# Performance work log

Hardware: AMD Instinct MI355X
Metric: run time of the kernel (lower is better)

## Reference

```python
import jax, jax.numpy as jnp
import numpy as np
import math

B, S, D, H, MAX_LEN = 4, 1024, 1024, 16, 1024
DH = D // H  # 64

def setup_inputs() -> dict:
    key = jax.random.key(0)
    ks = jax.random.split(key, 9)
    s = 1.0 / math.sqrt(D)
    return {
        "q":  jax.random.normal(ks[0], (B, S, D), jnp.float32),
        "kv": jax.random.normal(ks[1], (B, S, D), jnp.float32),
        "Wq": jax.random.normal(ks[2], (D, D), jnp.float32) * s,
        "bq": jax.random.normal(ks[3], (D,), jnp.float32) * s,
        "Wk": jax.random.normal(ks[4], (D, D), jnp.float32) * s,
        "bk": jax.random.normal(ks[5], (D,), jnp.float32) * s,
        "Wv": jax.random.normal(ks[6], (D, D), jnp.float32) * s,
        "bv": jax.random.normal(ks[7], (D,), jnp.float32) * s,
        "Er": jax.random.normal(ks[8], (MAX_LEN, DH), jnp.float32),
    }

def _skew(QEr):
    # QEr: [B, H, S, S]. Music-Transformer skew trick:
    # pad one zero column on the left, reshape, drop first row.
    b, h, r, c = QEr.shape
    padded = jnp.pad(QEr, ((0, 0), (0, 0), (0, 0), (1, 0)))  # [b,h,r,c+1]
    reshaped = padded.reshape(b, h, c + 1, r)
    return reshaped[:, :, 1:, :]  # [b,h,r,c]

def reference(q, kv, Wq, bq, Wk, bk, Wv, bv, Er):
    b, s, d = kv.shape
    # projections (nn.Linear: x @ W + b with W stored [in,out])
    k = (kv @ Wk + bk).reshape(b, s, H, DH).transpose(0, 2, 3, 1)  # [b,h,dh,s]
    v = (kv @ Wv + bv).reshape(b, s, H, DH).transpose(0, 2, 1, 3)  # [b,h,s,dh]
    qh = (q @ Wq + bq).reshape(b, s, H, DH).transpose(0, 2, 1, 3)  # [b,h,s,dh]
    # relative position scores
    Er_t = Er[MAX_LEN - s:, :].T            # [dh, s]
    QEr = jnp.einsum('bhsd,dt->bhst', qh, Er_t)
    Srel = _skew(QEr)                        # [b,h,s,s]
    # content scores
    QK = jnp.einsum('bhsd,bhdt->bhst', qh, k)
    attn = (QK + Srel) / math.sqrt(DH)
    causal = jnp.tril(jnp.ones((s, s), dtype=bool))[None, None]
    attn = jnp.where(causal, attn, -jnp.inf)
    attn = jax.nn.softmax(attn, axis=-1)
    out = jnp.einsum('bhst,bhtd->bhsd', attn, v)
    out = out.transpose(0, 2, 1, 3).reshape(b, s, d)
    return out  # dropout is identity (p=0 / eval)
```

## Files before the change

kernel.cpp:

```cpp
#include <hip/hip_runtime.h>
#include <hip/hip_bf16.h>

typedef __bf16 bf16x8 __attribute__((ext_vector_type(8)));
typedef __bf16 bf16x4 __attribute__((ext_vector_type(4)));
typedef float  f32x4  __attribute__((ext_vector_type(4)));

#define MFMA_B16(a, b, c) __builtin_amdgcn_mfma_f32_16x16x32_bf16((a), (b), (c), 0, 0, 0)

static constexpr int Bk  = 4;
static constexpr int Sk  = 1024;
static constexpr int Dk  = 1024;
static constexpr int Hk  = 16;
static constexpr int DHk = 64;

static constexpr size_t QH_OFF = 0;
static constexpr size_t K_OFF  = 4194304;
static constexpr size_t VT_OFF = 8388608;
static constexpr size_t WT_OFF = 12582912;
static constexpr size_t ER_OFF = 15728640;
static constexpr size_t WS_ELEMS = 15794176;

__device__ __forceinline__ void load_lds16(const void* g, void* l) {
    __builtin_amdgcn_global_load_lds((const __attribute__((address_space(1))) void*)g,
                                     (__attribute__((address_space(3))) void*)l, 16, 0, 0);
}

__global__ void prep_kernel(const float* __restrict__ Wq, const float* __restrict__ Wk,
                            const float* __restrict__ Wv, const float* __restrict__ Er,
                            __bf16* __restrict__ wt, __bf16* __restrict__ erb)
{
    __shared__ float tile[64][65];
    const int z = blockIdx.z;
    const int tid = threadIdx.x;
    if (z == 3) {
        int idx = (blockIdx.y * 16 + blockIdx.x) * 256 + tid;
        erb[idx] = (__bf16)Er[idx];
        return;
    }
    const float* W = (z == 0) ? Wq : (z == 1 ? Wk : Wv);
    __bf16* dst = wt + (size_t)z * Dk * Dk;
    const int k0 = blockIdx.y * 64, n0 = blockIdx.x * 64;
    #pragma unroll
    for (int j = 0; j < 16; ++j) {
        int idx = tid + j * 256; int r = idx >> 6, c = idx & 63;
        tile[r][c] = W[(size_t)(k0 + r) * Dk + n0 + c];
    }
    __syncthreads();
    #pragma unroll
    for (int j = 0; j < 16; ++j) {
        int idx = tid + j * 256; int r = idx >> 6, c = idx & 63;
        dst[(size_t)(n0 + r) * Dk + k0 + c] = (__bf16)tile[c][r];
    }
}

__global__ __launch_bounds__(256) void proj_kernel(
    const float* __restrict__ Xq, const float* __restrict__ Xkv,
    const float* __restrict__ bq, const float* __restrict__ bk,
    const float* __restrict__ bv, const __bf16* __restrict__ wt,
    __bf16* __restrict__ qh, __bf16* __restrict__ kws, __bf16* __restrict__ vt)
{
    __shared__ __align__(16) float  Al[128 * 32];
    __shared__ __align__(16) __bf16 Bl[128 * 32];

    const int z = blockIdx.z;
    const float* X    = (z == 0) ? Xq : Xkv;
    const float* bias = (z == 0) ? bq : (z == 1 ? bk : bv);
    const __bf16* Wz  = wt + (size_t)z * Dk * Dk;

    const int m0   = blockIdx.x * 128;
    const int n0   = blockIdx.y * 128;
    const int tid  = threadIdx.x;
    const int lane = tid & 63;
    const int w    = tid >> 6;
    const int wr   = w >> 1, wc = w & 1;
    const int l15  = lane & 15;
    const int g    = lane >> 4;

    const float* asrc[4];
    int adst[4];
    #pragma unroll
    for (int i = 0; i < 4; ++i) {
        const int c = w * 4 + i;
        asrc[i] = X + (size_t)(m0 + c * 8 + (lane >> 3)) * Dk + (((lane & 7) ^ (lane >> 3)) << 2);
        adst[i] = c * 1024 + lane * 16;
    }
    const __bf16* bsrc[2];
    int bdst[2];
    #pragma unroll
    for (int i = 0; i < 2; ++i) {
        const int c = w * 2 + i;
        bsrc[i] = Wz + (size_t)(n0 + c * 16 + (lane >> 2)) * Dk + (((lane & 3) ^ ((lane >> 3) & 3)) << 3);
        bdst[i] = c * 1024 + lane * 16;
    }

    int aoff0[4], aoff1[4], boff[4];
    #pragma unroll
    for (int m = 0; m < 4; ++m) {
        const int row = wr * 64 + m * 16 + l15;
        aoff0[m] = row * 128 + (((2 * g)     ^ (l15 & 7)) << 4);
        aoff1[m] = row * 128 + (((2 * g + 1) ^ (l15 & 7)) << 4);
    }
    #pragma unroll
    for (int n = 0; n < 4; ++n) {
        const int row = wc * 64 + n * 16 + l15;
        boff[n] = row * 64 + ((g ^ ((l15 >> 1) & 3)) << 4);
    }

    const f32x4 fz = {0.f, 0.f, 0.f, 0.f};
    f32x4 acc[4][4];
    #pragma unroll
    for (int m = 0; m < 4; ++m)
        #pragma unroll
        for (int n = 0; n < 4; ++n) acc[m][n] = fz;

    const char* Alc = (const char*)Al;
    const char* Blc = (const char*)Bl;

    for (int ks = 0; ks < Dk / 32; ++ks) {
        #pragma unroll
        for (int i = 0; i < 4; ++i)
            load_lds16(asrc[i], (char*)Al + adst[i]);
        #pragma unroll
        for (int i = 0; i < 2; ++i)
            load_lds16(bsrc[i], (char*)Bl + bdst[i]);
        #pragma unroll
        for (int i = 0; i < 4; ++i) asrc[i] += 32;
        #pragma unroll
        for (int i = 0; i < 2; ++i) bsrc[i] += 32;
        __syncthreads();

        bf16x8 bf[4];
        #pragma unroll
        for (int n = 0; n < 4; ++n)
            bf[n] = *(const bf16x8*)(Blc + boff[n]);
        bf16x8 af[4];
        #pragma unroll
        for (int m = 0; m < 4; ++m) {
            f32x4 x0 = *(const f32x4*)(Alc + aoff0[m]);
            f32x4 x1 = *(const f32x4*)(Alc + aoff1[m]);
            bf16x8 a;
            a[0] = (__bf16)x0[0]; a[1] = (__bf16)x0[1]; a[2] = (__bf16)x0[2]; a[3] = (__bf16)x0[3];
            a[4] = (__bf16)x1[0]; a[5] = (__bf16)x1[1]; a[6] = (__bf16)x1[2]; a[7] = (__bf16)x1[3];
            af[m] = a;
        }

        #pragma unroll
        for (int m = 0; m < 4; ++m)
            #pragma unroll
            for (int n = 0; n < 4; ++n)
                acc[m][n] = MFMA_B16(af[m], bf[n], acc[m][n]);
        __syncthreads();
    }

    #pragma unroll
    for (int n = 0; n < 4; ++n) {
        const float bb = bias[n0 + wc * 64 + n * 16 + l15];
        #pragma unroll
        for (int m = 0; m < 4; ++m)
            #pragma unroll
            for (int r = 0; r < 4; ++r) acc[m][n][r] += bb;
    }

    const int b   = m0 >> 10;
    const int s0t = (m0 & 1023) + wr * 64;
    const int h   = (n0 + wc * 64) >> 6;

    if (z < 2) {
        __bf16* dst = (z == 0) ? qh : kws;
        const size_t rowbase = (size_t)(b * Hk + h) * Sk;
        #pragma unroll
        for (int m = 0; m < 4; ++m) {
            #pragma unroll
            for (int r = 0; r < 4; ++r) {
                const int s = s0t + m * 16 + g * 4 + r;
                __bf16* drow = dst + (rowbase + s) * DHk;
                #pragma unroll
                for (int n = 0; n < 4; ++n)
                    drow[n * 16 + l15] = (__bf16)acc[m][n][r];
            }
        }
    } else {
        const size_t hb = (size_t)(b * Hk + h) * DHk;
        #pragma unroll
        for (int m = 0; m < 4; ++m) {
            const int sb = s0t + m * 16 + g * 4;
            #pragma unroll
            for (int n = 0; n < 4; ++n) {
                const int dh = n * 16 + l15;
                bf16x4 pk;
                #pragma unroll
                for (int r = 0; r < 4; ++r) pk[r] = (__bf16)acc[m][n][r];
                *(bf16x4*)(vt + (hb + dh) * Sk + sb) = pk;
            }
        }
    }
}

__global__ __launch_bounds__(256, 3) void attn_kernel(
    const __bf16* __restrict__ qh, const __bf16* __restrict__ kws,
    const __bf16* __restrict__ vt, const __bf16* __restrict__ erb,
    float* __restrict__ out)
{
    __shared__ __align__(16) __bf16 Kl[2][4096];
    __shared__ __align__(16) __bf16 Vl[2][4096];
    __shared__ __align__(16) __bf16 P_lds[4][16][88];

    const int tid  = threadIdx.x;
    const int lane = tid & 63;
    const int w    = tid >> 6;
    const int l15  = lane & 15;
    const int g    = lane >> 4;

    const int lid   = blockIdx.x;
    const int bh    = lid & 63;
    const int strip = 15 - (lid >> 6);
    const int ntw   = strip + 1;
    const int sw    = strip * 64 + w * 16;

    const __bf16* kbase = kws + (size_t)bh * Sk * DHk;
    const __bf16* vbase = vt  + (size_t)bh * DHk * Sk;
    const __bf16* qbase = qh  + ((size_t)bh * Sk + sw) * DHk;

    __bf16 (*Pw)[88] = P_lds[w];

    const int trow   = tid >> 3;
    const int tslot  = tid & 7;
    const int srcoff = (tslot ^ (trow & 7)) << 3;
    char* kd0 = (char*)Kl + tid * 16;
    char* vd0 = (char*)Vl + tid * 16;

    bf16x8 aq[2];
    aq[0] = *(const bf16x8*)(qbase + l15 * DHk + g * 8);
    aq[1] = *(const bf16x8*)(qbase + l15 * DHk + 32 + g * 8);

    const f32x4 fz = {0.f, 0.f, 0.f, 0.f};
    f32x4 O[4];
    float m_[4], l_[4];
    #pragma unroll
    for (int n = 0; n < 4; ++n) O[n] = fz;
    #pragma unroll
    for (int r = 0; r < 4; ++r) { m_[r] = -1e30f; l_[r] = 0.f; }

    load_lds16(kbase + (size_t)trow * DHk + srcoff,        kd0);
    load_lds16(kbase + (size_t)(32 + trow) * DHk + srcoff, kd0 + 4096);
    load_lds16(vbase + (size_t)trow * Sk + srcoff,         vd0);
    load_lds16(vbase + (size_t)(32 + trow) * Sk + srcoff,  vd0 + 4096);

    for (int it = 0; it < ntw; ++it) {
        const int t0  = it * 64;
        const int cur = it & 1;

        __builtin_amdgcn_sched_barrier(0);
        __builtin_amdgcn_s_barrier();
        __builtin_amdgcn_sched_barrier(0);
        if (it + 1 < ntw) {
            const int t0n = t0 + 64;
            char* kd = kd0 + (cur ^ 1) * 8192;
            char* vd = vd0 + (cur ^ 1) * 8192;
            load_lds16(kbase + (size_t)(t0n + trow) * DHk + srcoff,      kd);
            load_lds16(kbase + (size_t)(t0n + 32 + trow) * DHk + srcoff, kd + 4096);
            load_lds16(vbase + (size_t)trow * Sk + t0n + srcoff,         vd);
            load_lds16(vbase + (size_t)(32 + trow) * Sk + t0n + srcoff,  vd + 4096);
            asm volatile("s_waitcnt vmcnt(4)" ::: "memory");
        } else {
            asm volatile("s_waitcnt vmcnt(0)" ::: "memory");
        }
        __builtin_amdgcn_sched_barrier(0);
        __builtin_amdgcn_s_barrier();
        __builtin_amdgcn_sched_barrier(0);

        const char* Kc = (const char*)Kl + cur * 8192;
        const char* Vc = (const char*)Vl + cur * 8192;

        const int jb = t0 - sw + 1008;
        bf16x8 ec[10];
        #pragma unroll
        for (int kt = 0; kt < 2; ++kt)
            #pragma unroll
            for (int jj = 0; jj < 5; ++jj) {
                int jr = jb + jj * 16 + l15;
                jr = (jr > 1023) ? 1023 : jr;
                ec[kt * 5 + jj] = *(const bf16x8*)(erb + (size_t)jr * DHk + kt * 32 + g * 8);
            }

        f32x4 sc[4];
        #pragma unroll
        for (int j = 0; j < 4; ++j) sc[j] = fz;
        #pragma unroll
        for (int kt = 0; kt < 2; ++kt) {
            bf16x8 kb[4];
            #pragma unroll
            for (int j = 0; j < 4; ++j)
                kb[j] = *(const bf16x8*)(Kc + (j * 16 + l15) * 128 + ((((kt << 2) | g) ^ (l15 & 7)) << 4));
            __builtin_amdgcn_s_setprio(1);
            #pragma unroll
            for (int j = 0; j < 4; ++j)
                sc[j] = MFMA_B16(aq[kt], kb[j], sc[j]);
            __builtin_amdgcn_s_setprio(0);
        }

        f32x4 gf[5];
        #pragma unroll
        for (int jj = 0; jj < 5; ++jj) gf[jj] = fz;
        __builtin_amdgcn_s_setprio(1);
        #pragma unroll
        for (int kt = 0; kt < 2; ++kt)
            #pragma unroll
            for (int jj = 0; jj < 5; ++jj)
                gf[jj] = MFMA_B16(aq[kt], ec[kt * 5 + jj], gf[jj]);
        __builtin_amdgcn_s_setprio(0);

        #pragma unroll
        for (int r = 0; r < 4; ++r) {
            const int rr  = g * 4 + r;
            const int sft = 15 - rr;
            const int src = (g << 4) + ((l15 + sft) & 15);
            const bool hi = (l15 + sft) >= 16;
            float h[5];
            #pragma unroll
            for (int jj = 0; jj < 5; ++jj) h[jj] = __shfl(gf[jj][r], src);
            const int s = sw + rr;
            #pragma unroll
            for (int j = 0; j < 4; ++j) {
                float gval = hi ? h[j + 1] : h[j];
                float v = (sc[j][r] + gval) * 0.125f;
                int t = t0 + j * 16 + l15;
                sc[j][r] = (t > s) ? -1e30f : v;
            }
        }

        #pragma unroll
        for (int r = 0; r < 4; ++r) {
            float mt = fmaxf(fmaxf(sc[0][r], sc[1][r]), fmaxf(sc[2][r], sc[3][r]));
            #pragma unroll
            for (int off = 1; off < 16; off <<= 1) mt = fmaxf(mt, __shfl_xor(mt, off));
            float mnew = fmaxf(m_[r], mt);
            float scl  = __expf(m_[r] - mnew);
            float rsum = 0.f;
            #pragma unroll
            for (int j = 0; j < 4; ++j) {
                float p = __expf(sc[j][r] - mnew);
                sc[j][r] = p; rsum += p;
            }
            #pragma unroll
            for (int off = 1; off < 16; off <<= 1) rsum += __shfl_xor(rsum, off);
            l_[r] = l_[r] * scl + rsum;
            m_[r] = mnew;
            #pragma unroll
            for (int n = 0; n < 4; ++n) O[n][r] *= scl;
        }

        #pragma unroll
        for (int j = 0; j < 4; ++j)
            #pragma unroll
            for (int r = 0; r < 4; ++r)
                Pw[g * 4 + r][j * 16 + l15] = (__bf16)sc[j][r];
        __builtin_amdgcn_sched_barrier(0);

        __builtin_amdgcn_s_setprio(1);
        #pragma unroll
        for (int kt = 0; kt < 2; ++kt) {
            bf16x8 pa = *(const bf16x8*)(&Pw[l15][kt * 32 + g * 8]);
            #pragma unroll
            for (int n = 0; n < 4; ++n) {
                bf16x8 vbf = *(const bf16x8*)(Vc + (n * 16 + l15) * 128 + ((((kt << 2) | g) ^ (l15 & 7)) << 4));
                O[n] = MFMA_B16(pa, vbf, O[n]);
            }
        }
        __builtin_amdgcn_s_setprio(0);
    }

    const int b = bh >> 4, h = bh & 15;
    float* obase = out + ((size_t)b * Sk + sw) * Dk + h * DHk;
    #pragma unroll
    for (int r = 0; r < 4; ++r) {
        float inv = 1.f / l_[r];
        #pragma unroll
        for (int n = 0; n < 4; ++n)
            obase[(size_t)(g * 4 + r) * Dk + n * 16 + l15] = O[n][r] * inv;
    }
}

extern "C" void kernel_launch(void* const* d_in, const int* in_sizes, int n_in,
                              void* d_out, int out_size, void* d_ws, size_t ws_size,
                              hipStream_t stream)
{
    const float* q  = (const float*)d_in[0];
    const float* kv = (const float*)d_in[1];
    const float* Wq = (const float*)d_in[2];
    const float* bq = (const float*)d_in[3];
    const float* Wk = (const float*)d_in[4];
    const float* bk = (const float*)d_in[5];
    const float* Wv = (const float*)d_in[6];
    const float* bv = (const float*)d_in[7];
    const float* Er = (const float*)d_in[8];
    float* out = (float*)d_out;

    if (ws_size < WS_ELEMS * sizeof(__bf16)) return;
    __bf16* ws  = (__bf16*)d_ws;
    __bf16* qh  = ws + QH_OFF;
    __bf16* kws = ws + K_OFF;
    __bf16* vt  = ws + VT_OFF;
    __bf16* wt  = ws + WT_OFF;
    __bf16* erb = ws + ER_OFF;

    prep_kernel<<<dim3(16, 16, 4), 256, 0, stream>>>(Wq, Wk, Wv, Er, wt, erb);
    proj_kernel<<<dim3(32, 8, 3), 256, 0, stream>>>(q, kv, bq, bk, bv, wt, qh, kws, vt);
    attn_kernel<<<dim3(1024), 256, 0, stream>>>(qh, kws, vt, erb, out);
}
```

Before: 104.7 us.

## Use exp2 softmax with lazy rescale, DPP reductions, and packed bf16 P stores

```diff
diff --git a/kernel.cpp b/kernel.cpp
--- a/kernel.cpp
+++ b/kernel.cpp
@@ -4,6 +4,7 @@
 typedef __bf16 bf16x8 __attribute__((ext_vector_type(8)));
 typedef __bf16 bf16x4 __attribute__((ext_vector_type(4)));
 typedef float  f32x4  __attribute__((ext_vector_type(4)));
+typedef unsigned __attribute__((may_alias)) u32a;
 
 #define MFMA_B16(a, b, c) __builtin_amdgcn_mfma_f32_16x16x32_bf16((a), (b), (c), 0, 0, 0)
 
@@ -23,6 +24,32 @@
 __device__ __forceinline__ void load_lds16(const void* g, void* l) {
     __builtin_amdgcn_global_load_lds((const __attribute__((address_space(1))) void*)g,
                                      (__attribute__((address_space(3))) void*)l, 16, 0, 0);
+}
+
+template<int CTRL>
+__device__ __forceinline__ float dppf(float x) {
+    int v = __builtin_bit_cast(int, x);
+    return __builtin_bit_cast(float,
+        __builtin_amdgcn_update_dpp(v, v, CTRL, 0xF, 0xF, false));
+}
+__device__ __forceinline__ float rmax16(float x) {
+    x = fmaxf(x, dppf<0x128>(x));
+    x = fmaxf(x, dppf<0x124>(x));
+    x = fmaxf(x, dppf<0x122>(x));
+    x = fmaxf(x, dppf<0x121>(x));
+    return x;
+}
+__device__ __forceinline__ float rsum16(float x) {
+    x += dppf<0x128>(x);
+    x += dppf<0x124>(x);
+    x += dppf<0x122>(x);
+    x += dppf<0x121>(x);
+    return x;
+}
+__device__ __forceinline__ unsigned pk_bf16(float lo, float hi) {
+    unsigned r;
+    asm("v_cvt_pk_bf16_f32 %0, %1, %2" : "=v"(r) : "v"(lo), "v"(hi));
+    return r;
 }
 
 __global__ void prep_kernel(const float* __restrict__ Wq, const float* __restrict__ Wk,
@@ -240,6 +267,8 @@
     for (int n = 0; n < 4; ++n) O[n] = fz;
     #pragma unroll
     for (int r = 0; r < 4; ++r) { m_[r] = -1e30f; l_[r] = 0.f; }
+
+    const float SCL = 0.125f * 1.44269504088896f;
 
     load_lds16(kbase + (size_t)trow * DHk + srcoff,        kd0);
     load_lds16(kbase + (size_t)(32 + trow) * DHk + srcoff, kd0 + 4096);
@@ -323,38 +352,60 @@
             #pragma unroll
             for (int j = 0; j < 4; ++j) {
                 float gval = hi ? h[j + 1] : h[j];
-                float v = (sc[j][r] + gval) * 0.125f;
+                float v = (sc[j][r] + gval) * SCL;
                 int t = t0 + j * 16 + l15;
                 sc[j][r] = (t > s) ? -1e30f : v;
             }
         }
 
+        float mt[4];
+        #pragma unroll
+        for (int r = 0; r < 4; ++r)
+            mt[r] = rmax16(fmaxf(fmaxf(sc[0][r], sc[1][r]), fmaxf(sc[2][r], sc[3][r])));
+
+        bool grow = (mt[0] > m_[0] + 8.f) || (mt[1] > m_[1] + 8.f) ||
+                    (mt[2] > m_[2] + 8.f) || (mt[3] > m_[3] + 8.f);
+        if (__any(grow)) {
+            #pragma unroll
+            for (int r = 0; r < 4; ++r) {
+                float mnew = fmaxf(m_[r], mt[r]);
+                float scl  = exp2f(m_[r] - mnew);
+                l_[r] *= scl;
+                m_[r]  = mnew;
+                #pragma unroll
+                for (int n = 0; n < 4; ++n) O[n][r] *= scl;
+            }
+        }
         #pragma unroll
         for (int r = 0; r < 4; ++r) {
-            float mt = fmaxf(fmaxf(sc[0][r], sc[1][r]), fmaxf(sc[2][r], sc[3][r]));
-            #pragma unroll
-            for (int off = 1; off < 16; off <<= 1) mt = fmaxf(mt, __shfl_xor(mt, off));
-            float mnew = fmaxf(m_[r], mt);
-            float scl  = __expf(m_[r] - mnew);
-            float rsum = 0.f;
+            float rs = 0.f;
             #pragma unroll
             for (int j = 0; j < 4; ++j) {
-                float p = __expf(sc[j][r] - mnew);
-                sc[j][r] = p; rsum += p;
-            }
-            #pragma unroll
-            for (int off = 1; off < 16; off <<= 1) rsum += __shfl_xor(rsum, off);
-            l_[r] = l_[r] * scl + rsum;
-            m_[r] = mnew;
-            #pragma unroll
-            for (int n = 0; n < 4; ++n) O[n][r] *= scl;
-        }
-
-        #pragma unroll
-        for (int j = 0; j < 4; ++j)
-            #pragma unroll
-            for (int r = 0; r < 4; ++r)
-                Pw[g * 4 + r][j * 16 + l15] = (__bf16)sc[j][r];
+                float p = exp2f(sc[j][r] - m_[r]);
+                sc[j][r] = p; rs += p;
+            }
+            l_[r] += rsum16(rs);
+        }
+
+        {
+            const int p01 = l15 & 1;
+            #pragma unroll
+            for (int j = 0; j < 4; ++j) {
+                #pragma unroll
+                for (int h2 = 0; h2 < 2; ++h2) {
+                    float a0 = sc[j][h2];
+                    float a2 = sc[j][h2 + 2];
+                    float b0 = dppf<0xB1>(a0);
+                    float b2 = dppf<0xB1>(a2);
+                    float lo = p01 ? b2 : a0;
+                    float hi = p01 ? a2 : b0;
+                    unsigned wd = pk_bf16(lo, hi);
+                    const int row = g * 4 + h2 + (p01 ? 2 : 0);
+                    *(u32a*)(&Pw[row][(j << 4) + (l15 & ~1)]) = wd;
+                }
+            }
+        }
+        asm volatile("" ::: "memory");
         __builtin_amdgcn_sched_barrier(0);
 
         __builtin_amdgcn_s_setprio(1);
```

Result: no change. 103.4 us (-1.2%).
